# Optimization experiments

Hardware: AMD Instinct MI355X
Metric: run time of the kernel (lower is better)

The kernel has to match this reference:

```python
import jax, jax.numpy as jnp
import numpy as np

N, F, H, O, D = 4096, 128, 4, 64, 64


def setup_inputs() -> dict:
    key = jax.random.key(0)
    k1, k2, k3, k4, k5 = jax.random.split(key, 5)
    h = jax.random.normal(k1, (1, N, F), dtype=jnp.float32)
    # dense binary adjacency (0/1)
    a = jax.random.randint(k2, (1, N, N), 0, 2).astype(jnp.float32)
    kernel = jax.random.normal(k3, (H, F, O), dtype=jnp.float32) * 0.1
    attn_kernel = jax.random.normal(k4, (H, F, D), dtype=jnp.float32) * 0.1
    attn_kernel2 = jax.random.normal(k5, (H, F, D), dtype=jnp.float32) * 0.1
    return {"h": h, "a": a, "kernel": kernel, "attn_kernel": attn_kernel, "attn_kernel2": attn_kernel2}


def reference(h, a, kernel, attn_kernel, attn_kernel2):
    x = h[0]          # [N, F]
    adj = a[0]        # [N, N] dense 0/1 adjacency
    # per-head linear projections, vectorized over heads
    feats = jnp.einsum('nf,hfo->hno', x, kernel)          # [H, N, O]
    f_self = jnp.einsum('nf,hfd->hnd', x, attn_kernel)    # [H, N, D]
    f_other = jnp.einsum('nf,hfd->hnd', x, attn_kernel2)  # [H, N, D]
    # dense attention logits, masked BEFORE the nonlinearity (as in original)
    dense = jnp.einsum('hnd,hmd->hnm', f_self, f_other)   # [H, N, N]
    masked = adj[None] * dense
    masked = jnp.where(masked >= 0, masked, 0.2 * masked)  # LeakyReLU(0.2)
    masked = masked / jnp.sqrt(jnp.asarray(D, jnp.float32))
    neg_inf = jnp.where(adj == 0, jnp.float32(-1e9), jnp.float32(0.0))  # [N, N]
    att = jax.nn.softmax(masked + neg_inf[None], axis=-1)
    att = att * (adj != 0).astype(att.dtype)[None]
    # aggregation (dropout is identity at inference, rate=0)
    node_features = jnp.einsum('hnm,hmo->hno', att, feats)  # [H, N, O]
    node_features = jax.nn.relu(node_features)
    # zero out padding rows (all-zero input features)
    row_mask = (jnp.sum((x != 0).astype(jnp.float32), axis=-1, keepdims=True) > 0).astype(jnp.float32)  # [N, 1]
    node_features = node_features * row_mask[None]
    # concat heads along last dim -> [1, N, H*O]
    out = jnp.transpose(node_features, (1, 0, 2)).reshape(N, H * O)
    return out[None]
```

## Files before the change

kernel.cpp:

```cpp
#include <hip/hip_runtime.h>
#include <hip/hip_bf16.h>

typedef unsigned short u16;
typedef unsigned int u32;
typedef unsigned long long u64;
typedef __attribute__((ext_vector_type(8))) short bf16x8;
typedef __attribute__((ext_vector_type(4))) float f32x4;
typedef __attribute__((ext_vector_type(4))) u16 u16x4;

#define N 4096
#define F 128
#define H 4
#define O 64
#define NW (N / 64)
#define NT 16
#define QSCALE 0.18033688011112043f

__device__ inline float exp2_hw(float x) {
#if __has_builtin(__builtin_amdgcn_exp2f)
  return __builtin_amdgcn_exp2f(x);
#else
  return __expf(x * 0.6931471805599453f);
#endif
}

__device__ inline u16 f2bf(float f) {
  union { __hip_bfloat16 b; u16 u; } v;
  v.b = __float2bfloat16(f);
  return v.u;
}

__global__ __launch_bounds__(256) void prep_kernel(
    const float* __restrict__ x, const float* __restrict__ adj,
    const float* __restrict__ wv, const float* __restrict__ wq,
    const float* __restrict__ wk, u16* __restrict__ Q, u16* __restrict__ K,
    u16* __restrict__ Vt, float* __restrict__ rmask, u64* __restrict__ bits) {
  const int b = blockIdx.x;
  const int t = threadIdx.x;

  if (b < 1024) {
    const int w = t >> 6, l = t & 63;
    const int row = b * 4 + w;
    const float* ar = adj + (size_t)row * N;
    u64* br = bits + (size_t)row * NW;
#pragma unroll 4
    for (int j2 = 0; j2 < 16; j2++) {
      float4 v = *(const float4*)&ar[j2 * 256 + l * 4];
      unsigned nib = (unsigned)(v.x != 0.f) | ((unsigned)(v.y != 0.f) << 1) |
                     ((unsigned)(v.z != 0.f) << 2) | ((unsigned)(v.w != 0.f) << 3);
      u64 word = (u64)nib << ((l & 15) * 4);
      word |= __shfl_xor(word, 1);
      word |= __shfl_xor(word, 2);
      word |= __shfl_xor(word, 4);
      word |= __shfl_xor(word, 8);
      if ((l & 15) == 0) br[j2 * 4 + (l >> 4)] = word;
    }
  } else if (b < 1792) {
    __shared__ __align__(16) u16 xb[64][136];
    __shared__ __align__(16) u16 wt[64][136];
    const int pb = b - 1024;
    const int brow = (pb & 63) * 64;
    const int p = pb >> 6, h = p / 3, which = p % 3;
    const float* W = (which == 0 ? wq : which == 1 ? wk : wv) + h * F * O;

#pragma unroll
    for (int i = 0; i < 8; i++) {
      int idx = t + i * 256, r = idx >> 5, c4 = idx & 31;
      float4 v = *(const float4*)&x[(brow + r) * F + c4 * 4];
      u16x4 o4 = { f2bf(v.x), f2bf(v.y), f2bf(v.z), f2bf(v.w) };
      *(u16x4*)&xb[r][c4 * 4] = o4;
    }
#pragma unroll
    for (int i = 0; i < 8; i++) {
      int idx = t + i * 256, k = idx >> 4, n4 = idx & 15;
      float4 v = *(const float4*)&W[k * O + n4 * 4];
      wt[n4 * 4 + 0][k] = f2bf(v.x);
      wt[n4 * 4 + 1][k] = f2bf(v.y);
      wt[n4 * 4 + 2][k] = f2bf(v.z);
      wt[n4 * 4 + 3][k] = f2bf(v.w);
    }
    __syncthreads();

    const int w = t >> 6, l = t & 63;
    const int lm = l & 15, lg = l >> 4;
    const f32x4 z4 = {0.f, 0.f, 0.f, 0.f};
    bf16x8 af[4];
#pragma unroll
    for (int kc = 0; kc < 4; kc++)
      af[kc] = *(const bf16x8*)&xb[w * 16 + lm][kc * 32 + lg * 8];
    f32x4 acc[4];
#pragma unroll
    for (int ct = 0; ct < 4; ct++) {
      acc[ct] = z4;
#pragma unroll
      for (int kc = 0; kc < 4; kc++) {
        bf16x8 bfr = *(const bf16x8*)&wt[ct * 16 + lm][kc * 32 + lg * 8];
        acc[ct] = __builtin_amdgcn_mfma_f32_16x16x32_bf16(af[kc], bfr, acc[ct], 0, 0, 0);
      }
    }

    const int orow = brow + w * 16 + lg * 4;
    if (which == 0) {
      u16* dst = Q + h * N * O;
#pragma unroll
      for (int ct = 0; ct < 4; ct++)
#pragma unroll
        for (int r = 0; r < 4; r++)
          dst[(orow + r) * O + ct * 16 + lm] = f2bf(acc[ct][r] * QSCALE);
    } else if (which == 1) {
      u16* dst = K + h * N * O;
#pragma unroll
      for (int ct = 0; ct < 4; ct++)
#pragma unroll
        for (int r = 0; r < 4; r++)
          dst[(orow + r) * O + ct * 16 + lm] = f2bf(acc[ct][r]);
    } else {
      u16* dst = Vt + h * O * N;
#pragma unroll
      for (int ct = 0; ct < 4; ct++) {
        u16x4 v4 = { f2bf(acc[ct][0]), f2bf(acc[ct][1]),
                     f2bf(acc[ct][2]), f2bf(acc[ct][3]) };
        *(u16x4*)&dst[(size_t)(ct * 16 + lm) * N + orow] = v4;
      }
    }
  } else {
    int n = (b - 1792) * 256 + t;
    const float4* xr = (const float4*)(x + n * F);
    float s = 0.f;
#pragma unroll
    for (int i = 0; i < F / 4; i++) {
      float4 v = xr[i];
      s += fabsf(v.x) + fabsf(v.y) + fabsf(v.z) + fabsf(v.w);
    }
    rmask[n] = (s != 0.f) ? 1.f : 0.f;
  }
}

__global__ __launch_bounds__(512) void attn_kernel(
    const u64* __restrict__ bits, const u16* __restrict__ Qg,
    const u16* __restrict__ Kg, const u16* __restrict__ Vtg,
    float* __restrict__ Opart, float* __restrict__ Spart) {
  __shared__ __align__(16) char kv[2][4][8192];
  __shared__ __align__(16) u16 pst[8][16][64];

  const int tid = threadIdx.x;
  const int w = tid >> 6, l = tid & 63;
  const int lm = l & 15, lg = l >> 4;
  const int rg = w >> 1, hc = w & 1;
  const int h = blockIdx.y;
  const int z = blockIdx.z;
  const int R0 = blockIdx.x * 64;
  const int WR0 = R0 + rg * 16;
  const int CB0 = z * 2048;

  const char* Kb = (const char*)(Kg + h * N * O);
  const char* Vb = (const char*)(Vtg + h * O * N);
  const u64* bblk = bits + (size_t)WR0 * NW;

  const int srow = w * 8 + (l >> 3);
  const int scol = ((l & 7) * 16) ^ ((srow & 7) << 4);

  const u16* Qh = Qg + h * N * O;
  bf16x8 qa0 = *(const bf16x8*)&Qh[(WR0 + lm) * O + lg * 8];
  bf16x8 qa1 = *(const bf16x8*)&Qh[(WR0 + lm) * O + 32 + lg * 8];

  bf16x8 ones;
#pragma unroll
  for (int i = 0; i < 8; i++) ones[i] = (short)0x3F80;

  char* pbase = (char*)&pst[w][0][0];
  const char* prd0 = pbase + lm * 128 + ((lg * 16) ^ ((lm & 7) << 4));
  const char* prd1 = pbase + lm * 128 + ((64 + lg * 16) ^ ((lm & 7) << 4));

  f32x4 oacc[4];
  f32x4 lacc = {0.f, 0.f, 0.f, 0.f};
#pragma unroll
  for (int i = 0; i < 4; i++) oacc[i] = (f32x4){0.f, 0.f, 0.f, 0.f};
  const f32x4 zero4 = {0.f, 0.f, 0.f, 0.f};

  auto STAGE = [&](int b, int t) {
    __builtin_amdgcn_global_load_lds(
        (const u32*)(Kb + (size_t)(CB0 + 0 * 1024 + t * 64 + srow) * 128 + scol),
        (u32*)&kv[b][0][w * 1024], 16, 0, 0);
    __builtin_amdgcn_global_load_lds(
        (const u32*)(Kb + (size_t)(CB0 + 1 * 1024 + t * 64 + srow) * 128 + scol),
        (u32*)&kv[b][1][w * 1024], 16, 0, 0);
    __builtin_amdgcn_global_load_lds(
        (const u32*)(Vb + (size_t)srow * (N * 2) + (CB0 + 0 * 1024 + t * 64) * 2 + scol),
        (u32*)&kv[b][2][w * 1024], 16, 0, 0);
    __builtin_amdgcn_global_load_lds(
        (const u32*)(Vb + (size_t)srow * (N * 2) + (CB0 + 1 * 1024 + t * 64) * 2 + scol),
        (u32*)&kv[b][3][w * 1024], 16, 0, 0);
  };

  STAGE(0, 0);
  __syncthreads();

  int b = 0;
#pragma unroll 1
  for (int t = 0; t < NT; ++t) {
    if (t + 1 < NT) STAGE(b ^ 1, t + 1);

    const int widx = (CB0 >> 6) + hc * NT + t;

    u64 sh0 = bblk[(lg * 4 + 0) * NW + widx] >> lm;
    u64 sh1 = bblk[(lg * 4 + 1) * NW + widx] >> lm;
    u64 sh2 = bblk[(lg * 4 + 2) * NW + widx] >> lm;
    u64 sh3 = bblk[(lg * 4 + 3) * NW + widx] >> lm;

    const char* Kt = &kv[b][hc][0];
    f32x4 sacc[4];
    __builtin_amdgcn_s_setprio(1);
#pragma unroll
    for (int tt = 0; tt < 4; tt++) {
      const int row = tt * 16 + lm;
      const int sw = (row & 7) << 4;
      bf16x8 kb0 = *(const bf16x8*)(Kt + row * 128 + ((lg * 16) ^ sw));
      bf16x8 kb1 = *(const bf16x8*)(Kt + row * 128 + ((lg * 16 + 64) ^ sw));
      f32x4 s0 = __builtin_amdgcn_mfma_f32_16x16x32_bf16(qa0, kb0, zero4, 0, 0, 0);
      sacc[tt] = __builtin_amdgcn_mfma_f32_16x16x32_bf16(qa1, kb1, s0, 0, 0, 0);
    }
    __builtin_amdgcn_s_setprio(0);

#pragma unroll
    for (int tt = 0; tt < 4; tt++) {
#pragma unroll
      for (int r = 0; r < 4; r++) {
        u64 sh = (r == 0 ? sh0 : r == 1 ? sh1 : r == 2 ? sh2 : sh3);
        unsigned bit = (unsigned)(sh >> (tt * 16)) & 1u;
        float sv = sacc[tt][r];
        float lv = fmaxf(sv, 0.2f * sv);
        float p = bit ? exp2_hw(lv) : 0.f;
        const int prow = lg * 4 + r;
        *(u16*)(pbase + prow * 128 +
                ((((tt * 16 + lm) * 2)) ^ ((prow & 7) << 4))) = f2bf(p);
      }
    }
    bf16x8 pa0 = *(const bf16x8*)prd0;
    bf16x8 pa1 = *(const bf16x8*)prd1;

    const char* Vt_ = &kv[b][2 + hc][0];
    __builtin_amdgcn_s_setprio(1);
#pragma unroll
    for (int ot = 0; ot < 4; ot++) {
      const int o = ot * 16 + lm;
      const int sw = (o & 7) << 4;
      bf16x8 vb0 = *(const bf16x8*)(Vt_ + o * 128 + ((lg * 16) ^ sw));
      bf16x8 vb1 = *(const bf16x8*)(Vt_ + o * 128 + ((lg * 16 + 64) ^ sw));
      oacc[ot] = __builtin_amdgcn_mfma_f32_16x16x32_bf16(pa0, vb0, oacc[ot], 0, 0, 0);
      oacc[ot] = __builtin_amdgcn_mfma_f32_16x16x32_bf16(pa1, vb1, oacc[ot], 0, 0, 0);
    }
    lacc = __builtin_amdgcn_mfma_f32_16x16x32_bf16(pa0, ones, lacc, 0, 0, 0);
    lacc = __builtin_amdgcn_mfma_f32_16x16x32_bf16(pa1, ones, lacc, 0, 0, 0);
    __builtin_amdgcn_s_setprio(0);

    __syncthreads();
    b ^= 1;
  }

  float (*Om2)[64][64] = (float (*)[64][64])&kv[0][0][0];
#pragma unroll
  for (int ot = 0; ot < 4; ot++)
#pragma unroll
    for (int r = 0; r < 4; r++)
      Om2[hc][rg * 16 + lg * 4 + r][ot * 16 + lm] = oacc[ot][r];
  if (lm == 0) {
    float* ps = (float*)pbase;
#pragma unroll
    for (int r = 0; r < 4; r++) ps[lg * 4 + r] = lacc[r];
  }
  __syncthreads();

  const int row = tid >> 3;
  const int c0 = (tid & 7) * 8;
  const int grow = R0 + row;
  float* op = &Opart[(((size_t)z * H + h) * N + grow) * O + c0];
#pragma unroll
  for (int j = 0; j < 8; j++)
    op[j] = Om2[0][row][c0 + j] + Om2[1][row][c0 + j];
  if ((tid & 7) == 0) {
    const int rg2 = row >> 4, ri = row & 15;
    float s0 = ((float*)&pst[rg2 * 2 + 0][0][0])[ri];
    float s1 = ((float*)&pst[rg2 * 2 + 1][0][0])[ri];
    Spart[((size_t)z * H + h) * N + grow] = s0 + s1;
  }
}

__global__ __launch_bounds__(256) void merge_kernel(
    const float* __restrict__ Opart, const float* __restrict__ Spart,
    const float* __restrict__ rowmask, float* __restrict__ out) {
  const int h = blockIdx.y;
  const int idx = blockIdx.x * 256 + threadIdx.x;
  const int row = idx >> 4, c0 = (idx & 15) * 4;
  float S = Spart[(size_t)h * N + row] + Spart[((size_t)H + h) * N + row];
  float inv = (S > 0.f) ? 1.f / S : 0.f;
  float rm = rowmask[row];
  const float4 o0 = *(const float4*)&Opart[((size_t)h * N + row) * O + c0];
  const float4 o1 = *(const float4*)&Opart[(((size_t)H + h) * N + row) * O + c0];
  float4 r;
  r.x = fmaxf((o0.x + o1.x) * inv, 0.f) * rm;
  r.y = fmaxf((o0.y + o1.y) * inv, 0.f) * rm;
  r.z = fmaxf((o0.z + o1.z) * inv, 0.f) * rm;
  r.w = fmaxf((o0.w + o1.w) * inv, 0.f) * rm;
  *(float4*)&out[(size_t)row * (H * O) + h * O + c0] = r;
}

extern "C" void kernel_launch(void* const* d_in, const int* in_sizes, int n_in,
                              void* d_out, int out_size, void* d_ws, size_t ws_size,
                              hipStream_t stream) {
  const float* x   = (const float*)d_in[0];
  const float* adj = (const float*)d_in[1];
  const float* wv  = (const float*)d_in[2];
  const float* wq  = (const float*)d_in[3];
  const float* wk  = (const float*)d_in[4];
  float* out = (float*)d_out;

  u16* Q  = (u16*)d_ws;
  u16* K  = Q + H * N * O;
  u16* Vt = K + H * N * O;
  float* rmask = (float*)(Vt + H * N * O);
  u64* bits = (u64*)(rmask + N);
  float* Opart = (float*)(bits + (size_t)N * NW);
  float* Spart = Opart + (size_t)2 * H * N * O;

  prep_kernel<<<dim3(1808), 256, 0, stream>>>(x, adj, wv, wq, wk, Q, K, Vt, rmask, bits);
  attn_kernel<<<dim3(N / 64, H, 2), 512, 0, stream>>>(bits, Q, K, Vt, Opart, Spart);
  merge_kernel<<<dim3(N * O / 4 / 256, H), 256, 0, stream>>>(Opart, Spart, rmask, out);
}
```

Baseline: 69.05 us.

## Keep attention probabilities in registers via transposed MFMA operand layout

Swaps the MFMA operand order so S is computed transposed and its output fragment matches the A/B input layout of the P·V MFMA. This lets P be packed into bf16 registers directly instead of round-tripping through shared memory. K rows are permuted and the LDS swizzle is adjusted to match, and the mask bits now come from a single 64-bit load per lane. It also adds a launch_bounds occupancy hint and pads the final reduction buffer. The risks are correctness of the row permutation and register pressure under the new occupancy bound.

```diff
diff --git a/kernel.cpp b/kernel.cpp
--- a/kernel.cpp
+++ b/kernel.cpp
@@ -136,12 +136,12 @@
   }
 }
 
-__global__ __launch_bounds__(512) void attn_kernel(
+__global__ __launch_bounds__(512, 4) void attn_kernel(
     const u64* __restrict__ bits, const u16* __restrict__ Qg,
     const u16* __restrict__ Kg, const u16* __restrict__ Vtg,
     float* __restrict__ Opart, float* __restrict__ Spart) {
   __shared__ __align__(16) char kv[2][4][8192];
-  __shared__ __align__(16) u16 pst[8][16][64];
+  __shared__ float Ss2[8][16];
 
   const int tid = threadIdx.x;
   const int w = tid >> 6, l = tid & 63;
@@ -158,7 +158,12 @@
   const u64* bblk = bits + (size_t)WR0 * NW;
 
   const int srow = w * 8 + (l >> 3);
-  const int scol = ((l & 7) * 16) ^ ((srow & 7) << 4);
+  const int ssw = (((srow & 3) | (((srow >> 3) & 1) << 2)) << 4);
+  const int scol = ((l & 7) * 16) ^ ssw;
+
+  const int krow_base = (lm & 3) + 8 * (lm >> 2);
+  const int ksw = (lm & 7) << 4;
+  const int vsw = (((lm & 3) | (((lm >> 3) & 1) << 2)) << 4);
 
   const u16* Qh = Qg + h * N * O;
   bf16x8 qa0 = *(const bf16x8*)&Qh[(WR0 + lm) * O + lg * 8];
@@ -167,10 +172,6 @@
   bf16x8 ones;
 #pragma unroll
   for (int i = 0; i < 8; i++) ones[i] = (short)0x3F80;
-
-  char* pbase = (char*)&pst[w][0][0];
-  const char* prd0 = pbase + lm * 128 + ((lg * 16) ^ ((lm & 7) << 4));
-  const char* prd1 = pbase + lm * 128 + ((64 + lg * 16) ^ ((lm & 7) << 4));
 
   f32x4 oacc[4];
   f32x4 lacc = {0.f, 0.f, 0.f, 0.f};
@@ -203,72 +204,65 @@
 
     const int widx = (CB0 >> 6) + hc * NT + t;
 
-    u64 sh0 = bblk[(lg * 4 + 0) * NW + widx] >> lm;
-    u64 sh1 = bblk[(lg * 4 + 1) * NW + widx] >> lm;
-    u64 sh2 = bblk[(lg * 4 + 2) * NW + widx] >> lm;
-    u64 sh3 = bblk[(lg * 4 + 3) * NW + widx] >> lm;
+    u64 word = bblk[lm * NW + widx];
+    u64 w2 = word >> (8 * lg);
 
     const char* Kt = &kv[b][hc][0];
     f32x4 sacc[4];
     __builtin_amdgcn_s_setprio(1);
 #pragma unroll
     for (int tt = 0; tt < 4; tt++) {
-      const int row = tt * 16 + lm;
-      const int sw = (row & 7) << 4;
-      bf16x8 kb0 = *(const bf16x8*)(Kt + row * 128 + ((lg * 16) ^ sw));
-      bf16x8 kb1 = *(const bf16x8*)(Kt + row * 128 + ((lg * 16 + 64) ^ sw));
-      f32x4 s0 = __builtin_amdgcn_mfma_f32_16x16x32_bf16(qa0, kb0, zero4, 0, 0, 0);
-      sacc[tt] = __builtin_amdgcn_mfma_f32_16x16x32_bf16(qa1, kb1, s0, 0, 0, 0);
+      const int row = krow_base + 4 * (tt & 1) + 32 * (tt >> 1);
+      bf16x8 kb0 = *(const bf16x8*)(Kt + row * 128 + ((lg * 16) ^ ksw));
+      bf16x8 kb1 = *(const bf16x8*)(Kt + row * 128 + ((lg * 16 + 64) ^ ksw));
+      f32x4 s0 = __builtin_amdgcn_mfma_f32_16x16x32_bf16(kb0, qa0, zero4, 0, 0, 0);
+      sacc[tt] = __builtin_amdgcn_mfma_f32_16x16x32_bf16(kb1, qa1, s0, 0, 0, 0);
     }
     __builtin_amdgcn_s_setprio(0);
 
+    float pv[4][4];
 #pragma unroll
     for (int tt = 0; tt < 4; tt++) {
 #pragma unroll
       for (int r = 0; r < 4; r++) {
-        u64 sh = (r == 0 ? sh0 : r == 1 ? sh1 : r == 2 ? sh2 : sh3);
-        unsigned bit = (unsigned)(sh >> (tt * 16)) & 1u;
+        unsigned bit = (unsigned)(w2 >> (4 * (tt & 1) + 32 * (tt >> 1) + r)) & 1u;
         float sv = sacc[tt][r];
         float lv = fmaxf(sv, 0.2f * sv);
-        float p = bit ? exp2_hw(lv) : 0.f;
-        const int prow = lg * 4 + r;
-        *(u16*)(pbase + prow * 128 +
-                ((((tt * 16 + lm) * 2)) ^ ((prow & 7) << 4))) = f2bf(p);
+        pv[tt][r] = bit ? exp2_hw(lv) : 0.f;
       }
     }
-    bf16x8 pa0 = *(const bf16x8*)prd0;
-    bf16x8 pa1 = *(const bf16x8*)prd1;
+    bf16x8 pa0, pa1;
+#pragma unroll
+    for (int r = 0; r < 4; r++) {
+      pa0[r]     = (short)f2bf(pv[0][r]);
+      pa0[4 + r] = (short)f2bf(pv[1][r]);
+      pa1[r]     = (short)f2bf(pv[2][r]);
+      pa1[4 + r] = (short)f2bf(pv[3][r]);
+    }
 
     const char* Vt_ = &kv[b][2 + hc][0];
     __builtin_amdgcn_s_setprio(1);
 #pragma unroll
     for (int ot = 0; ot < 4; ot++) {
       const int o = ot * 16 + lm;
-      const int sw = (o & 7) << 4;
-      bf16x8 vb0 = *(const bf16x8*)(Vt_ + o * 128 + ((lg * 16) ^ sw));
-      bf16x8 vb1 = *(const bf16x8*)(Vt_ + o * 128 + ((lg * 16 + 64) ^ sw));
-      oacc[ot] = __builtin_amdgcn_mfma_f32_16x16x32_bf16(pa0, vb0, oacc[ot], 0, 0, 0);
-      oacc[ot] = __builtin_amdgcn_mfma_f32_16x16x32_bf16(pa1, vb1, oacc[ot], 0, 0, 0);
-    }
-    lacc = __builtin_amdgcn_mfma_f32_16x16x32_bf16(pa0, ones, lacc, 0, 0, 0);
-    lacc = __builtin_amdgcn_mfma_f32_16x16x32_bf16(pa1, ones, lacc, 0, 0, 0);
+      bf16x8 vb0 = *(const bf16x8*)(Vt_ + o * 128 + ((lg * 16) ^ vsw));
+      bf16x8 vb1 = *(const bf16x8*)(Vt_ + o * 128 + ((lg * 16 + 64) ^ vsw));
+      oacc[ot] = __builtin_amdgcn_mfma_f32_16x16x32_bf16(vb0, pa0, oacc[ot], 0, 0, 0);
+      oacc[ot] = __builtin_amdgcn_mfma_f32_16x16x32_bf16(vb1, pa1, oacc[ot], 0, 0, 0);
+    }
+    lacc = __builtin_amdgcn_mfma_f32_16x16x32_bf16(ones, pa0, lacc, 0, 0, 0);
+    lacc = __builtin_amdgcn_mfma_f32_16x16x32_bf16(ones, pa1, lacc, 0, 0, 0);
     __builtin_amdgcn_s_setprio(0);
 
     __syncthreads();
     b ^= 1;
   }
 
-  float (*Om2)[64][64] = (float (*)[64][64])&kv[0][0][0];
+  float (*Om2)[64][68] = (float (*)[64][68])&kv[0][0][0];
 #pragma unroll
   for (int ot = 0; ot < 4; ot++)
-#pragma unroll
-    for (int r = 0; r < 4; r++)
-      Om2[hc][rg * 16 + lg * 4 + r][ot * 16 + lm] = oacc[ot][r];
-  if (lm == 0) {
-    float* ps = (float*)pbase;
-#pragma unroll
-    for (int r = 0; r < 4; r++) ps[lg * 4 + r] = lacc[r];
-  }
+    *(f32x4*)&Om2[hc][rg * 16 + lm][ot * 16 + lg * 4] = oacc[ot];
+  if (lg == 0) Ss2[w][lm] = lacc[0];
   __syncthreads();
 
   const int row = tid >> 3;
@@ -280,9 +274,7 @@
     op[j] = Om2[0][row][c0 + j] + Om2[1][row][c0 + j];
   if ((tid & 7) == 0) {
     const int rg2 = row >> 4, ri = row & 15;
-    float s0 = ((float*)&pst[rg2 * 2 + 0][0][0])[ri];
-    float s1 = ((float*)&pst[rg2 * 2 + 1][0][0])[ri];
-    Spart[((size_t)z * H + h) * N + grow] = s0 + s1;
+    Spart[((size_t)z * H + h) * N + grow] = Ss2[rg2 * 2 + 0][ri] + Ss2[rg2 * 2 + 1][ri];
   }
 }
 
```

Result: faster. 67.44 us (-2.3%).
